# Performance work log

Hardware: AMD Instinct MI355X
Metric: run time of the kernel (lower is better)

## Reference

```python
import jax, jax.numpy as jnp
import numpy as np
from jax import lax

V_PATCH_NUMS = (1, 2, 3, 4, 5, 6, 8, 10, 13, 16)
SHARE_K = 4
RESI = 0.5  # abs(quant_resi)


def _area_matrix(pn, H):
    # F.interpolate(mode='area') == adaptive_avg_pool2d: uniform mean over [floor, ceil) window
    W = np.zeros((pn, H), np.float32)
    for i in range(pn):
        s = int(np.floor(i * H / pn)); e = int(np.ceil((i + 1) * H / pn))
        W[i, s:e] = 1.0 / (e - s)
    return W


def _cubic(x, a=-0.75):
    x = abs(x)
    if x <= 1.0:
        return (a + 2) * x**3 - (a + 3) * x**2 + 1
    if x < 2.0:
        return a * x**3 - 5 * a * x**2 + 8 * a * x - 4 * a
    return 0.0


def _bicubic_matrix(out, inp):
    # torch bicubic, align_corners=False, a=-0.75, border-clamped (separable 1D matrix)
    W = np.zeros((out, inp), np.float32)
    for i in range(out):
        src = (i + 0.5) * inp / out - 0.5
        i0 = int(np.floor(src)); t = src - i0
        for k in range(-1, 3):
            j = min(max(i0 + k, 0), inp - 1)
            W[i, j] += _cubic(k - t)
    return W


def _phi_select(si, SN, K=SHARE_K):
    ticks = np.linspace(1 / 3 / K, 1 - 1 / 3 / K, K) if K == 4 else np.linspace(1 / 2 / K, 1 - 1 / 2 / K, K)
    return int(np.argmin(np.abs(ticks - si / (SN - 1))))


def _phi(h, w, b):
    # Phi: h*(1-r) + conv3x3(h)*r
    y = lax.conv_general_dilated(h, w, (1, 1), 'SAME',
                                 dimension_numbers=('NCHW', 'OIHW', 'NCHW'))
    y = y + b[None, :, None, None]
    return h * (1.0 - RESI) + y * RESI


def reference(f, embedding, phi_w, phi_b):
    # Multi-scale residual vector quantization (VectorQuantizer2 hot path).
    # f: [B, C, 16, 16] latent; embedding: [V, C]; phi_w: [K, C, C, 3, 3]; phi_b: [K, C]
    B, C, H, Wd = f.shape
    SN = len(V_PATCH_NUMS)
    e2 = jnp.sum(embedding**2, axis=1)  # [V]
    f_hat = jnp.zeros_like(f)
    f_rest = f
    for si, pn in enumerate(V_PATCH_NUMS):
        if si != SN - 1:
            A = jnp.asarray(_area_matrix(pn, H))
            z = jnp.einsum('ph,bchw,qw->bcpq', A, f_rest, A)  # area downsample to pn x pn
        else:
            z = f_rest
        zf = z.transpose(0, 2, 3, 1).reshape(-1, C)  # [B*pn*pn, C]
        # squared-distance cdist + argmin codebook lookup
        d = jnp.sum(zf**2, axis=1, keepdims=True) - 2.0 * (zf @ embedding.T) + e2[None, :]
        idx = jnp.argmin(d, axis=1)  # [B*pn*pn]
        h = embedding[idx].reshape(B, pn, pn, C).transpose(0, 3, 1, 2)  # gather -> [B,C,pn,pn]
        if si != SN - 1:
            U = jnp.asarray(_bicubic_matrix(H, pn))
            h = jnp.einsum('hp,bcpq,wq->bchw', U, h, U)  # bicubic upsample to H x W
        k = _phi_select(si, SN)
        h = _phi(h, phi_w[k], phi_b[k])  # partially-shared Phi residual refinement
        f_hat = f_hat + h
        f_rest = f_rest - h
    return f_hat


def setup_inputs() -> dict:
    key = jax.random.key(0)
    k1, k2, k3 = jax.random.split(key, 3)
    f = jax.random.normal(k1, (64, 32, 16, 16), dtype=jnp.float32)
    embedding = jax.random.normal(k2, (4096, 32), dtype=jnp.float32)
    phi_w = jax.random.normal(k3, (4, 32, 32, 3, 3), dtype=jnp.float32) * 0.05
    phi_b = jnp.zeros((4, 32), dtype=jnp.float32)
    return {"f": f, "embedding": embedding, "phi_w": phi_w, "phi_b": phi_b}
```

## Files before the change

kernel.cpp:

```cpp
#include <hip/hip_runtime.h>
#include <cmath>


#define BB 64
#define CC 32
#define HH 16
#define VV 4096
#define NTOT (BB*CC*HH*HH)
#define ABASE 163840
#define ATOT  42624

typedef __attribute__((ext_vector_type(8))) short bf16x8;
typedef __attribute__((ext_vector_type(4))) float f32x4;

__device__ __forceinline__ double cubicw(double x) {
    x = fabs(x);
    const double a = -0.75;
    if (x <= 1.0) return ((a + 2.0) * x - (a + 3.0)) * x * x + 1.0;
    if (x < 2.0)  return (((a * x - 5.0 * a) * x + 8.0 * a) * x - 4.0 * a);
    return 0.0;
}

__device__ __forceinline__ unsigned int ordf(float d) {
    unsigned int b = __float_as_uint(d);
    return (b & 0x80000000u) ? ~b : (b | 0x80000000u);
}

__device__ __forceinline__ short f2bf(float x) {
    unsigned u = __float_as_uint(x);
    unsigned r = (u + 0x7fffu + ((u >> 16) & 1u)) >> 16;
    return (short)r;
}
__device__ __forceinline__ float bf2f(short h) {
    return __uint_as_float(((unsigned)(unsigned short)h) << 16);
}

__global__ void init_k(const float* __restrict__ f, const float* __restrict__ E,
                       float* __restrict__ f_rest,
                       float* __restrict__ e2, float* __restrict__ z,
                       unsigned short* __restrict__ est,
                       unsigned long long* __restrict__ bka) {
    int i = blockIdx.x * 256 + threadIdx.x;
    if (i < NTOT) f_rest[i] = f[i];
    if (bka && i < ATOT) bka[i] = ~0ull;
    if (i < VV) {
        float s = 0.f;
        int tile = i >> 4, n = i & 15;
        #pragma unroll
        for (int c = 0; c < CC; ++c) {
            float x = E[i * CC + c];
            s += x * x;
            if (est) {
                short h = f2bf(x); float rm = x - bf2f(h);
                short m = f2bf(rm); float rl = rm - bf2f(m);
                short l = f2bf(rl);
                int idx = tile * 1536 + (n * 4 + (c >> 3)) * 8 + (c & 7);
                est[idx]        = (unsigned short)h;
                est[idx + 512]  = (unsigned short)m;
                est[idx + 1024] = (unsigned short)l;
            }
        }
        e2[i] = s;
    }
    if (i < BB * CC) {
        const float* src = f + (size_t)i * (HH * HH);
        float s = 0.f;
        for (int j = 0; j < HH * HH; ++j) s += src[j];
        z[i] = s * (1.0f / 256.0f);
    }
}

__global__ __launch_bounds__(256, 4) void argsmall_k(const float* __restrict__ z,
        const float* __restrict__ E, const float* __restrict__ e2,
        unsigned long long* __restrict__ bestk, int M, int G, int gsz) {
    const int t = threadIdx.x;
    int m = blockIdx.x * 64 + (t & 63);
    int w = __builtin_amdgcn_readfirstlane(t >> 6);
    int wg = blockIdx.y * 4 + w;
    int v0 = wg * gsz;
    float zr[CC]; float z2 = 0.f;
    const float4* zp = (const float4*)(z + (size_t)m * CC);
    #pragma unroll
    for (int c4 = 0; c4 < 8; ++c4) {
        float4 v = zp[c4];
        zr[c4*4+0] = v.x; zr[c4*4+1] = v.y; zr[c4*4+2] = v.z; zr[c4*4+3] = v.w;
        z2 += v.x*v.x + v.y*v.y + v.z*v.z + v.w*v.w;
    }
    const float* e = E + (size_t)v0 * CC;
    float best = 3.4e38f; int bv = v0;
    for (int v = v0; v < v0 + gsz; v += 2, e += 2 * CC) {
        float a0 = 0.f, a1 = 0.f, b0 = 0.f, b1 = 0.f;
        #pragma unroll
        for (int c = 0; c < CC; c += 2) {
            a0 = fmaf(zr[c],   e[c],      a0);
            a1 = fmaf(zr[c+1], e[c+1],    a1);
            b0 = fmaf(zr[c],   e[CC+c],   b0);
            b1 = fmaf(zr[c+1], e[CC+c+1], b1);
        }
        float dA = fmaf(-2.f, a0 + a1, z2 + e2[v]);
        float dB = fmaf(-2.f, b0 + b1, z2 + e2[v+1]);
        if (dA < best) { best = dA; bv = v; }
        if (dB < best) { best = dB; bv = v + 1; }
    }
    bestk[(size_t)m * G + wg] = ((unsigned long long)ordf(best) << 32) |
                                (unsigned long long)(unsigned int)bv;
}

__global__ __launch_bounds__(256, 4) void argmf_k(const unsigned short* __restrict__ zs,
        const unsigned short* __restrict__ est, const float* __restrict__ e2,
        unsigned long long* __restrict__ bka, int M, int G, int gsz) {
    const int t = threadIdx.x;
    const int g = blockIdx.y;
    const int v0 = g * gsz;
    const int lane = t & 63;
    const int w = t >> 6;
    const int n = lane & 15, kq = lane >> 4;

    int tb[2]; bf16x8 ah[2], am[2], al[2];
    #pragma unroll
    for (int pt = 0; pt < 2; ++pt) {
        int tb0 = blockIdx.x * 128 + w * 32 + pt * 16;
        if (tb0 > M - 16) tb0 = M - 16;
        tb[pt] = tb0;
        const unsigned short* zp = zs + (size_t)(tb0 + n) * 96 + kq * 8;
        ah[pt] = *(const bf16x8*)(zp);
        am[pt] = *(const bf16x8*)(zp + 32);
        al[pt] = *(const bf16x8*)(zp + 64);
    }

    float bd[2][4]; int bc[2][4];
    #pragma unroll
    for (int pt = 0; pt < 2; ++pt)
        #pragma unroll
        for (int r = 0; r < 4; ++r) { bd[pt][r] = 3.4e38f; bc[pt][r] = 0; }

    const int nct = gsz >> 4;
    const unsigned short* ep = est + (size_t)(v0 >> 4) * 1536 +
                               (size_t)(n * 4 + kq) * 8;
    const float* e2p = e2 + v0 + n;
    bf16x8 eh = *(const bf16x8*)(ep);
    bf16x8 em = *(const bf16x8*)(ep + 512);
    bf16x8 el = *(const bf16x8*)(ep + 1024);
    float e2c = *e2p;
    for (int ct = 0; ct < nct; ++ct) {
        bf16x8 ceh = eh, cem = em, cel = el; float ce2 = e2c;
        if (ct + 1 < nct) {
            ep += 1536; e2p += 16;
            eh = *(const bf16x8*)(ep);
            em = *(const bf16x8*)(ep + 512);
            el = *(const bf16x8*)(ep + 1024);
            e2c = *e2p;
        }
        #pragma unroll
        for (int pt = 0; pt < 2; ++pt) {
            f32x4 Ca = {0.f, 0.f, 0.f, 0.f};
            f32x4 Cb = {ce2, ce2, ce2, ce2};
            Ca = __builtin_amdgcn_mfma_f32_16x16x32_bf16(ah[pt], ceh, Ca, 0, 0, 0);
            Cb = __builtin_amdgcn_mfma_f32_16x16x32_bf16(am[pt], ceh, Cb, 0, 0, 0);
            Ca = __builtin_amdgcn_mfma_f32_16x16x32_bf16(ah[pt], cem, Ca, 0, 0, 0);
            Cb = __builtin_amdgcn_mfma_f32_16x16x32_bf16(al[pt], ceh, Cb, 0, 0, 0);
            Ca = __builtin_amdgcn_mfma_f32_16x16x32_bf16(ah[pt], cel, Ca, 0, 0, 0);
            Cb = __builtin_amdgcn_mfma_f32_16x16x32_bf16(am[pt], cem, Cb, 0, 0, 0);
            #pragma unroll
            for (int r = 0; r < 4; ++r) {
                float d = Ca[r] + Cb[r];
                if (d < bd[pt][r]) { bd[pt][r] = d; bc[pt][r] = ct; }
            }
        }
    }
    #pragma unroll
    for (int pt = 0; pt < 2; ++pt) {
        #pragma unroll
        for (int r = 0; r < 4; ++r) {
            int v = v0 + bc[pt][r] * 16 + n;
            unsigned long long k = ((unsigned long long)ordf(bd[pt][r]) << 32) |
                                   (unsigned long long)(unsigned int)v;
            #pragma unroll
            for (int msk = 1; msk < 16; msk <<= 1) {
                unsigned long long o = __shfl_xor(k, msk);
                if (o < k) k = o;
            }
            if (n == 0)
                atomicMin(&bka[(size_t)(tb[pt] + kq * 4 + r)], k);
        }
    }
}

__global__ __launch_bounds__(256, 2) void argmf4_k(const unsigned short* __restrict__ zs,
        const unsigned short* __restrict__ est, const float* __restrict__ e2,
        unsigned long long* __restrict__ bka, int M, int G, int gsz) {
    const int t = threadIdx.x;
    const int g = blockIdx.y;
    const int v0 = g * gsz;
    const int lane = t & 63;
    const int w = t >> 6;
    const int n = lane & 15, kq = lane >> 4;

    int tb[4]; bf16x8 ah[4], am[4], al[4];
    #pragma unroll
    for (int pt = 0; pt < 4; ++pt) {
        int tb0 = blockIdx.x * 256 + w * 64 + pt * 16;
        if (tb0 > M - 16) tb0 = M - 16;
        tb[pt] = tb0;
        const unsigned short* zp = zs + (size_t)(tb0 + n) * 96 + kq * 8;
        ah[pt] = *(const bf16x8*)(zp);
        am[pt] = *(const bf16x8*)(zp + 32);
        al[pt] = *(const bf16x8*)(zp + 64);
    }

    float bd[4][4]; int bc[4][4];
    #pragma unroll
    for (int pt = 0; pt < 4; ++pt)
        #pragma unroll
        for (int r = 0; r < 4; ++r) { bd[pt][r] = 3.4e38f; bc[pt][r] = 0; }

    const int nct = gsz >> 4;
    const unsigned short* ep = est + (size_t)(v0 >> 4) * 1536 +
                               (size_t)(n * 4 + kq) * 8;
    const float* e2p = e2 + v0 + n;
    bf16x8 eh = *(const bf16x8*)(ep);
    bf16x8 em = *(const bf16x8*)(ep + 512);
    bf16x8 el = *(const bf16x8*)(ep + 1024);
    float e2c = *e2p;
    for (int ct = 0; ct < nct; ++ct) {
        bf16x8 ceh = eh, cem = em, cel = el; float ce2 = e2c;
        if (ct + 1 < nct) {
            ep += 1536; e2p += 16;
            eh = *(const bf16x8*)(ep);
            em = *(const bf16x8*)(ep + 512);
            el = *(const bf16x8*)(ep + 1024);
            e2c = *e2p;
        }
        #pragma unroll
        for (int pt = 0; pt < 4; ++pt) {
            f32x4 Ca = {0.f, 0.f, 0.f, 0.f};
            f32x4 Cb = {ce2, ce2, ce2, ce2};
            Ca = __builtin_amdgcn_mfma_f32_16x16x32_bf16(ah[pt], ceh, Ca, 0, 0, 0);
            Cb = __builtin_amdgcn_mfma_f32_16x16x32_bf16(am[pt], ceh, Cb, 0, 0, 0);
            Ca = __builtin_amdgcn_mfma_f32_16x16x32_bf16(ah[pt], cem, Ca, 0, 0, 0);
            Cb = __builtin_amdgcn_mfma_f32_16x16x32_bf16(al[pt], ceh, Cb, 0, 0, 0);
            Ca = __builtin_amdgcn_mfma_f32_16x16x32_bf16(ah[pt], cel, Ca, 0, 0, 0);
            Cb = __builtin_amdgcn_mfma_f32_16x16x32_bf16(am[pt], cem, Cb, 0, 0, 0);
            #pragma unroll
            for (int r = 0; r < 4; ++r) {
                float d = Ca[r] + Cb[r];
                if (d < bd[pt][r]) { bd[pt][r] = d; bc[pt][r] = ct; }
            }
        }
    }
    #pragma unroll
    for (int pt = 0; pt < 4; ++pt) {
        #pragma unroll
        for (int r = 0; r < 4; ++r) {
            int v = v0 + bc[pt][r] * 16 + n;
            unsigned long long k = ((unsigned long long)ordf(bd[pt][r]) << 32) |
                                   (unsigned long long)(unsigned int)v;
            #pragma unroll
            for (int msk = 1; msk < 16; msk <<= 1) {
                unsigned long long o = __shfl_xor(k, msk);
                if (o < k) k = o;
            }
            if (n == 0)
                atomicMin(&bka[(size_t)(tb[pt] + kq * 4 + r)], k);
        }
    }
}

__global__ __launch_bounds__(256, 4) void argbig_k(const float* __restrict__ z,
        const float* __restrict__ E, const float* __restrict__ e2,
        unsigned long long* __restrict__ bestk, int M, int G, int gsz) {
    __shared__ float s_e[128 * CC];
    __shared__ float s_e2[128];
    const int T = gridDim.x * 256;
    const int g = blockIdx.y;
    const int v0 = g * gsz;
    {
        const float4* src = (const float4*)(E + (size_t)v0 * CC);
        float4* dst = (float4*)s_e;
        for (int i = threadIdx.x; i < gsz * 8; i += 256) dst[i] = src[i];
        if (threadIdx.x < gsz) s_e2[threadIdx.x] = e2[v0 + threadIdx.x];
    }
    int   mm[2];
    bool  act[2];
    float zr[2][CC];
    float z2[2];
    #pragma unroll
    for (int pt = 0; pt < 2; ++pt) {
        int m0 = blockIdx.x * 256 + threadIdx.x + pt * T;
        act[pt] = (m0 < M);
        int m = act[pt] ? m0 : M - 1;
        mm[pt] = m;
        const float4* zp = (const float4*)(z + (size_t)m * CC);
        float zz = 0.f;
        #pragma unroll
        for (int c4 = 0; c4 < 8; ++c4) {
            float4 v = zp[c4];
            zr[pt][c4*4+0] = v.x; zr[pt][c4*4+1] = v.y;
            zr[pt][c4*4+2] = v.z; zr[pt][c4*4+3] = v.w;
            zz += v.x*v.x + v.y*v.y + v.z*v.z + v.w*v.w;
        }
        z2[pt] = zz;
    }
    __syncthreads();
    float best[2]; int bv[2];
    #pragma unroll
    for (int pt = 0; pt < 2; ++pt) { best[pt] = 3.4e38f; bv[pt] = v0; }
    const float4* ev = (const float4*)s_e;
    for (int vi = 0; vi < gsz; ++vi, ev += 8) {
        float4 e0 = ev[0], e1 = ev[1], e2v = ev[2], e3 = ev[3];
        float4 e4 = ev[4], e5 = ev[5], e6v = ev[6], e7 = ev[7];
        float ef[CC] = {e0.x,e0.y,e0.z,e0.w, e1.x,e1.y,e1.z,e1.w,
                        e2v.x,e2v.y,e2v.z,e2v.w, e3.x,e3.y,e3.z,e3.w,
                        e4.x,e4.y,e4.z,e4.w, e5.x,e5.y,e5.z,e5.w,
                        e6v.x,e6v.y,e6v.z,e6v.w, e7.x,e7.y,e7.z,e7.w};
        float a0 = 0.f, a1 = 0.f, b0 = 0.f, b1 = 0.f;
        #pragma unroll
        for (int c = 0; c < CC; c += 2) {
            a0 = fmaf(zr[0][c],   ef[c],   a0);
            a1 = fmaf(zr[0][c+1], ef[c+1], a1);
            b0 = fmaf(zr[1][c],   ef[c],   b0);
            b1 = fmaf(zr[1][c+1], ef[c+1], b1);
        }
        float e2c = s_e2[vi];
        float dA = fmaf(-2.f, a0 + a1, z2[0] + e2c);
        float dB = fmaf(-2.f, b0 + b1, z2[1] + e2c);
        int v = v0 + vi;
        if (dA < best[0]) { best[0] = dA; bv[0] = v; }
        if (dB < best[1]) { best[1] = dB; bv[1] = v; }
    }
    #pragma unroll
    for (int pt = 0; pt < 2; ++pt)
        if (act[pt])
            bestk[(size_t)mm[pt] * G + g] =
                ((unsigned long long)ordf(best[pt]) << 32) |
                (unsigned long long)(unsigned int)bv[pt];
}

__global__ __launch_bounds__(512) void fuse_k(const unsigned long long* __restrict__ bestk,
                      const float* __restrict__ E,
                      const float* __restrict__ pw, const float* __restrict__ pb,
                      const float* __restrict__ fsrc, float* __restrict__ fout,
                      float* __restrict__ f_rest,
                      float* __restrict__ z_next, unsigned short* __restrict__ zsn,
                      int pn, int G, int TPP, int kphi, int pnn) {
    __shared__ float s_buf[CC * 18 * 20];
    __shared__ float s_scratch[256 * 36];
    __shared__ float s_pw[CC * 3 * 4 * 8];
    __shared__ int   s_idx[256];
    __shared__ float s_w[HH][4];
    __shared__ int   s_j[HH][4];
    __shared__ unsigned long long s_red[256];
    const int t   = threadIdx.x;
    const int cog = blockIdx.x;
    const int b   = blockIdx.y;
    const int P   = pn * pn;
    const int half = t >> 8;
    const int tl   = t & 255;

    if (G == 0) {
        if (t < P)
            s_idx[t] = (int)(unsigned int)(bestk[(size_t)b * P + t] & 0xffffffffull);
    } else {
        int p = t / TPP, sub = t - p * TPP;
        unsigned long long bk = ~0ull;
        if (p < P) {
            const unsigned long long* kp = bestk + (size_t)(b * P + p) * G;
            for (int gg = sub; gg < G; gg += TPP) {
                unsigned long long o = kp[gg];
                if (o < bk) bk = o;
            }
        }
        int bfly = TPP > 64 ? 64 : TPP;
        for (int msk = 1; msk < bfly; msk <<= 1) {
            unsigned long long o = __shfl_xor(bk, msk);
            if (o < bk) bk = o;
        }
        if (p < P) {
            if (TPP <= 64) {
                if (sub == 0) s_red[p] = bk;
            } else {
                int K = TPP >> 6;
                if ((sub & 63) == 0) s_red[p * K + (sub >> 6)] = bk;
            }
        }
    }
    if (t < HH) {
        double src = (t + 0.5) * (double)pn / 16.0 - 0.5;
        double fi = floor(src); int i0 = (int)fi; double tt = src - fi;
        #pragma unroll
        for (int k = 0; k < 4; ++k) {
            int j = i0 - 1 + k; j = j < 0 ? 0 : (j > pn - 1 ? pn - 1 : j);
            s_j[t][k] = j;
            s_w[t][k] = (float)cubicw((double)(k - 1) - tt);
        }
    }
    {
        const float* src = pw + ((size_t)(kphi * CC + cog * 8)) * CC * 9;
        for (int i = t; i < 8 * CC * 9; i += 512) {
            int l  = i / (CC * 9);
            int r  = i - l * (CC * 9);
            int ci = r / 9; int kk = r - ci * 9;
            int kh = kk / 3; int kw = kk - kh * 3;
            int cp = l >> 1, ce = l & 1;
            s_pw[ci * 96 + kh * 32 + cp * 8 + ce * 4 + kw] = src[i];
        }
    }
    __syncthreads();
    if (G != 0 && t < P) {
        unsigned long long r = s_red[(TPP <= 64) ? t : t * (TPP >> 6)];
        if (TPP > 64) {
            int K = TPP >> 6;
            for (int j2 = 1; j2 < K; ++j2) {
                unsigned long long o = s_red[t * K + j2];
                if (o < r) r = o;
            }
        }
        s_idx[t] = (int)(unsigned int)(r & 0xffffffffull);
    }
    if (G != 0) __syncthreads();

    if (tl < HH * pn) {
        int h = tl / pn, q = tl % pn;
        int cbase = half * 16;
        float acc[16];
        #pragma unroll
        for (int c = 0; c < 16; ++c) acc[c] = 0.f;
        #pragma unroll
        for (int k = 0; k < 4; ++k) {
            float wv = s_w[h][k];
            if (wv == 0.0f) continue;
            int row = s_idx[s_j[h][k] * pn + q];
            const float4* er = (const float4*)(E + (size_t)row * CC + cbase);
            #pragma unroll
            for (int c4 = 0; c4 < 4; ++c4) {
                float4 e4 = er[c4];
                acc[c4*4+0] = fmaf(wv, e4.x, acc[c4*4+0]);
                acc[c4*4+1] = fmaf(wv, e4.y, acc[c4*4+1]);
                acc[c4*4+2] = fmaf(wv, e4.z, acc[c4*4+2]);
                acc[c4*4+3] = fmaf(wv, e4.w, acc[c4*4+3]);
            }
        }
        float* dst = &s_scratch[(h * pn + q) * 36 + cbase];
        *(float4*)(dst + 0)  = make_float4(acc[0],  acc[1],  acc[2],  acc[3]);
        *(float4*)(dst + 4)  = make_float4(acc[4],  acc[5],  acc[6],  acc[7]);
        *(float4*)(dst + 8)  = make_float4(acc[8],  acc[9],  acc[10], acc[11]);
        *(float4*)(dst + 12) = make_float4(acc[12], acc[13], acc[14], acc[15]);
    }
    __syncthreads();

    {
        int h = tl >> 4, w = tl & 15;
        int cbase = half * 16;
        float acc[16];
        #pragma unroll
        for (int c = 0; c < 16; ++c) acc[c] = 0.f;
        #pragma unroll
        for (int k = 0; k < 4; ++k) {
            float wh = s_w[w][k];
            int j = s_j[w][k];
            const float4* sp4 = (const float4*)&s_scratch[(h * pn + j) * 36 + cbase];
            float4 v0 = sp4[0], v1 = sp4[1], v2 = sp4[2], v3 = sp4[3];
            acc[0]  = fmaf(wh, v0.x, acc[0]);  acc[1]  = fmaf(wh, v0.y, acc[1]);
            acc[2]  = fmaf(wh, v0.z, acc[2]);  acc[3]  = fmaf(wh, v0.w, acc[3]);
            acc[4]  = fmaf(wh, v1.x, acc[4]);  acc[5]  = fmaf(wh, v1.y, acc[5]);
            acc[6]  = fmaf(wh, v1.z, acc[6]);  acc[7]  = fmaf(wh, v1.w, acc[7]);
            acc[8]  = fmaf(wh, v2.x, acc[8]);  acc[9]  = fmaf(wh, v2.y, acc[9]);
            acc[10] = fmaf(wh, v2.z, acc[10]); acc[11] = fmaf(wh, v2.w, acc[11]);
            acc[12] = fmaf(wh, v3.x, acc[12]); acc[13] = fmaf(wh, v3.y, acc[13]);
            acc[14] = fmaf(wh, v3.z, acc[14]); acc[15] = fmaf(wh, v3.w, acc[15]);
        }
        #pragma unroll
        for (int c = 0; c < 16; ++c)
            s_buf[((cbase + c) * 18 + h + 1) * 20 + w + 1] = acc[c];
        if (w == 0) {
            #pragma unroll
            for (int c = 0; c < 16; ++c) s_buf[((cbase + c) * 18 + h + 1) * 20] = 0.f;
        }
        if (w >= 13) {
            #pragma unroll
            for (int c = 0; c < 16; ++c) s_buf[((cbase + c) * 18 + h + 1) * 20 + w + 4] = 0.f;
        }
        if (h == 0) {
            #pragma unroll
            for (int c = 0; c < 16; ++c) {
                s_buf[((cbase + c) * 18) * 20 + w] = 0.f;
                if (w < 4) s_buf[((cbase + c) * 18) * 20 + 16 + w] = 0.f;
            }
        }
        if (h == 15) {
            #pragma unroll
            for (int c = 0; c < 16; ++c) {
                s_buf[((cbase + c) * 18 + 17) * 20 + w] = 0.f;
                if (w < 4) s_buf[((cbase + c) * 18 + 17) * 20 + 16 + w] = 0.f;
            }
        }
    }
    __syncthreads();

    const int wave = t >> 6;
    const int lane = t & 63;
    const int cp   = ((wave & 1) << 1) | (lane >> 5);
    const int s    = lane & 31;
    const int h    = s >> 1;
    const int w0   = (s & 1) * 8;
    const int wid  = wave >> 1;
    const int pos  = cp * 32 + s;
    const int stag = wave & 1;
    float accE[8], accO[8];
    #pragma unroll
    for (int o = 0; o < 8; ++o) { accE[o] = 0.f; accO[o] = 0.f; }
    const int ci0 = wid * 8;
    for (int ci = ci0; ci < ci0 + 8; ++ci) {
        const float* wrow = &s_pw[ci * 96 + cp * 8];
        #pragma unroll
        for (int kk = 0; kk < 3; ++kk) {
            int kh = kk + stag; kh = (kh >= 3) ? kh - 3 : kh;
            const float4* xr = (const float4*)&s_buf[(ci * 18 + h + kh) * 20 + w0];
            float4 a0 = xr[0], a1 = xr[1], a2 = xr[2];
            float xf[12] = {a0.x, a0.y, a0.z, a0.w, a1.x, a1.y, a1.z, a1.w,
                            a2.x, a2.y, a2.z, a2.w};
            const float4* wp = (const float4*)(wrow + kh * 32);
            float4 wA = wp[0];
            float4 wB = wp[1];
            #pragma unroll
            for (int o = 0; o < 8; ++o) {
                accE[o] += xf[o] * wA.x + xf[o+1] * wA.y + xf[o+2] * wA.z;
                accO[o] += xf[o] * wB.x + xf[o+1] * wB.y + xf[o+2] * wB.z;
            }
        }
    }
    if (wid != 0) {
        float* dst = &s_scratch[((wid - 1) * 128 + pos) * 20];
        *(float4*)(dst +  0) = make_float4(accE[0], accE[1], accE[2], accE[3]);
        *(float4*)(dst +  4) = make_float4(accE[4], accE[5], accE[6], accE[7]);
        *(float4*)(dst +  8) = make_float4(accO[0], accO[1], accO[2], accO[3]);
        *(float4*)(dst + 12) = make_float4(accO[4], accO[5], accO[6], accO[7]);
    }
    __syncthreads();

    float4 rE0, rE1, rO0, rO1;
    if (wid == 0) {
        #pragma unroll
        for (int g2 = 0; g2 < 3; ++g2) {
            const float* sp = &s_scratch[(g2 * 128 + pos) * 20];
            float4 p0 = *(const float4*)(sp + 0), p1 = *(const float4*)(sp + 4);
            float4 p2 = *(const float4*)(sp + 8), p3 = *(const float4*)(sp + 12);
            accE[0] += p0.x; accE[1] += p0.y; accE[2] += p0.z; accE[3] += p0.w;
            accE[4] += p1.x; accE[5] += p1.y; accE[6] += p1.z; accE[7] += p1.w;
            accO[0] += p2.x; accO[1] += p2.y; accO[2] += p2.z; accO[3] += p2.w;
            accO[4] += p3.x; accO[5] += p3.y; accO[6] += p3.z; accO[7] += p3.w;
        }
        float biasE = pb[kphi * CC + cog * 8 + cp * 2];
        float biasO = pb[kphi * CC + cog * 8 + cp * 2 + 1];
        #pragma unroll
        for (int o = 0; o < 8; ++o) { accE[o] += biasE; accO[o] += biasO; }
        #pragma unroll
        for (int c = 0; c < 2; ++c) {
            const float* acc = c ? accO : accE;
            int co = cog * 8 + cp * 2 + c;
            float hf[8];
            #pragma unroll
            for (int o = 0; o < 8; ++o) {
                float hv = s_buf[(co * 18 + h + 1) * 20 + w0 + o + 1];
                hf[o] = 0.5f * hv + 0.5f * acc[o];
            }
            size_t base = ((size_t)(b * CC + co) * HH + h) * HH + w0;
            float4* fr = (float4*)(f_rest + base);
            float4 r0 = fr[0], r1 = fr[1];
            r0.x -= hf[0]; r0.y -= hf[1]; r0.z -= hf[2]; r0.w -= hf[3];
            r1.x -= hf[4]; r1.y -= hf[5]; r1.z -= hf[6]; r1.w -= hf[7];
            if (pnn > 0) {
                fr[0] = r0; fr[1] = r1;
            } else {
                const float4* fs = (const float4*)(fsrc + base);
                float4 s0 = fs[0], s1 = fs[1];
                float4 o0, o1;
                o0.x = s0.x - r0.x; o0.y = s0.y - r0.y;
                o0.z = s0.z - r0.z; o0.w = s0.w - r0.w;
                o1.x = s1.x - r1.x; o1.y = s1.y - r1.y;
                o1.z = s1.z - r1.z; o1.w = s1.w - r1.w;
                float4* fo = (float4*)(fout + base);
                fo[0] = o0; fo[1] = o1;
            }
            if (c) { rO0 = r0; rO1 = r1; } else { rE0 = r0; rE1 = r1; }
        }
    }

    if (pnn > 0) {
        __syncthreads();
        float* fn = s_buf;
        if (wid == 0) {
            #pragma unroll
            for (int c = 0; c < 2; ++c) {
                int cl = cp * 2 + c;
                float* d = &fn[(cl * HH + h) * HH + w0];
                float4 r0 = c ? rO0 : rE0, r1 = c ? rO1 : rE1;
                d[0] = r0.x; d[1] = r0.y; d[2] = r0.z; d[3] = r0.w;
                d[4] = r1.x; d[5] = r1.y; d[6] = r1.z; d[7] = r1.w;
            }
        }
        __syncthreads();
        int P2 = pnn * pnn;
        for (int i = t; i < P2 * 8; i += 512) {
            int cl = i & 7, pq = i >> 3;
            int q2 = pq % pnn, p2 = pq / pnn;
            int sp = (p2 * HH) / pnn, ep = ((p2 + 1) * HH + pnn - 1) / pnn;
            int sq = (q2 * HH) / pnn, eq = ((q2 + 1) * HH + pnn - 1) / pnn;
            float wgt = 1.0f / ((float)(ep - sp) * (float)(eq - sq));
            float sum = 0.f;
            for (int h2 = sp; h2 < ep; ++h2)
                for (int w2 = sq; w2 < eq; ++w2)
                    sum += fn[(cl * HH + h2) * HH + w2];
            float v = sum * wgt;
            int c = cog * 8 + cl;
            if (zsn) {
                float tv = -2.0f * v;
                size_t baz = (size_t)(b * P2 + pq) * 96 + c;
                unsigned short hh = (unsigned short)f2bf(tv);
                float rm = tv - bf2f((short)hh);
                unsigned short mm2 = (unsigned short)f2bf(rm);
                float rl = rm - bf2f((short)mm2);
                unsigned short ll = (unsigned short)f2bf(rl);
                zsn[baz] = hh; zsn[baz + 32] = mm2; zsn[baz + 64] = ll;
            } else {
                z_next[((size_t)(b * P2 + pq)) * CC + c] = v;
            }
        }
    }
}

extern "C" void kernel_launch(void* const* d_in, const int* in_sizes, int n_in,
                              void* d_out, int out_size, void* d_ws, size_t ws_size,
                              hipStream_t stream) {
    const float* f  = (const float*)d_in[0];
    const float* E  = (const float*)d_in[1];
    const float* pw = (const float*)d_in[2];
    const float* pb = (const float*)d_in[3];
    float* out = (float*)d_out;

    const size_t need_base = (size_t)(NTOT + VV) * 4 + (size_t)524288 * 8 +
                             (size_t)524288 * 4;
    const size_t need_mf = need_base + (size_t)VV * 96 * 2 +
                           (size_t)16384 * 96 * 2;
    const bool use_mf = (ws_size >= need_mf);

    float* wsf    = (float*)d_ws;
    float* f_rest = wsf;
    float* e2     = wsf + (size_t)NTOT;
    unsigned long long* bestk = (unsigned long long*)(e2 + VV);
    float* z      = (float*)(bestk + 524288);
    unsigned short* est = use_mf ? (unsigned short*)(z + 524288) : (unsigned short*)0;
    unsigned short* zs  = use_mf ? (est + (size_t)VV * 96) : (unsigned short*)0;
    unsigned long long* bka = use_mf ? (bestk + ABASE) : (unsigned long long*)0;

    int phik[10];
    {
        double start = 1.0 / 3.0 / 4.0;
        double stop  = 1.0 - 1.0 / 3.0 / 4.0;
        double step  = (stop - start) / 3.0;
        double ticks[4];
        for (int i = 0; i < 4; ++i) ticks[i] = (double)i * step + start;
        ticks[3] = stop;
        for (int si = 0; si < 10; ++si) {
            double s = (double)si / 9.0;
            int bk = 0; double bd = fabs(ticks[0] - s);
            for (int tq = 1; tq < 4; ++tq) {
                double d2 = fabs(ticks[tq] - s);
                if (d2 < bd) { bd = d2; bk = tq; }
            }
            phik[si] = bk;
        }
    }

    static const int pns[10]  = {1, 2, 3, 4, 5, 6, 8, 10, 13, 16};
    static const int grpS[10] = {256, 128, 64, 32, 32, 16, 0, 0, 0, 0};
    static const int grpF[10] = {0, 0, 0, 0, 0, 0, 128, 64, 32, 32};
    static const int grpM[10] = {0, 0, 0, 32, 32, 32, 16, 16, 16, 16};
    static const int aoff[10] = {0, 0, 0, 0, 1024, 2624, 4928, 9024, 15424, 26240};

    init_k<<<(NTOT + 255) / 256, 256, 0, stream>>>(f, E, f_rest, e2, z, est, bka);

    for (int si = 0; si < 10; ++si) {
        int pn = pns[si];
        int P = pn * pn;
        int M = BB * P;
        int G, TPP;
        bool small_path = use_mf ? (pn <= 3) : (pn <= 6);
        const unsigned long long* fuse_bk = bestk;
        if (small_path) {
            int grp = grpS[si];
            G = grp * 4;
            int gsz = VV / G;
            argsmall_k<<<dim3(P, grp), 256, 0, stream>>>(z, E, e2, bestk, M, G, gsz);
            TPP = 1;
            while (TPP * 2 * P <= 512) TPP *= 2;
        } else if (use_mf) {
            int grp = grpM[si];
            int gsz = VV / grp;
            unsigned long long* slice = bka + aoff[si];
            if (pn >= 8) {
                int bx = (M + 255) / 256;
                argmf4_k<<<dim3(bx, grp), 256, 0, stream>>>(zs, est, e2, slice, M, grp, gsz);
            } else {
                int bx = (M + 127) / 128;
                argmf_k<<<dim3(bx, grp), 256, 0, stream>>>(zs, est, e2, slice, M, grp, gsz);
            }
            fuse_bk = slice;
            G = 0; TPP = 1;
        } else {
            G = grpF[si];
            int gsz = VV / G;
            int bx = (M + 511) / 512;
            argbig_k<<<dim3(bx, G), 256, 0, stream>>>(z, E, e2, bestk, M, G, gsz);
            TPP = 1;
            while (TPP * 2 * P <= 512) TPP *= 2;
        }
        int pnn = (si < 9) ? pns[si + 1] : 0;
        unsigned short* zsn = (pnn >= 4 && use_mf) ? zs : (unsigned short*)0;
        fuse_k<<<dim3(4, BB), 512, 0, stream>>>(fuse_bk, E, pw, pb,
                                                f, out, f_rest, z, zsn,
                                                pn, G, TPP, phik[si], pnn);
    }
}
```

Measured before the change: 363.7 us.

## Fuse small-scale codebook argmin into fuse kernel with ping-pong z buffers

For scales with pn<=4 on the MFMA path, the separate argmin kernel launch is dropped. The fuse kernel now computes full codebook distances itself, with each block scanning all 4096 entries per patch position and reducing with shuffles. The z buffer is split into two halves used alternately, so a fuse block can read the current z while writing the next scale's z. This removes several kernel launches and global round-trips. In exchange, each of the 4x64 fuse blocks redundantly evaluates the whole codebook, leaving the small-scale argmin with far less parallelism than the dedicated kernel had.

```diff
diff --git a/kernel.cpp b/kernel.cpp
--- a/kernel.cpp
+++ b/kernel.cpp
@@ -341,6 +341,7 @@
                       const float* __restrict__ pw, const float* __restrict__ pb,
                       const float* __restrict__ fsrc, float* __restrict__ fout,
                       float* __restrict__ f_rest,
+                      const float* __restrict__ z_in, const float* __restrict__ e2g,
                       float* __restrict__ z_next, unsigned short* __restrict__ zsn,
                       int pn, int G, int TPP, int kphi, int pnn) {
     __shared__ float s_buf[CC * 18 * 20];
@@ -360,6 +361,46 @@
     if (G == 0) {
         if (t < P)
             s_idx[t] = (int)(unsigned int)(bestk[(size_t)b * P + t] & 0xffffffffull);
+    } else if (G < 0) {
+        int p = t / TPP, sub = t - p * TPP;
+        unsigned long long bk = ~0ull;
+        if (p < P) {
+            float zr[CC]; float z2 = 0.f;
+            const float4* zp4 = (const float4*)(z_in + (size_t)(b * P + p) * CC);
+            #pragma unroll
+            for (int c4 = 0; c4 < 8; ++c4) {
+                float4 v4 = zp4[c4];
+                zr[c4*4+0] = v4.x; zr[c4*4+1] = v4.y;
+                zr[c4*4+2] = v4.z; zr[c4*4+3] = v4.w;
+                z2 += v4.x*v4.x + v4.y*v4.y + v4.z*v4.z + v4.w*v4.w;
+            }
+            const float* e = E + (size_t)sub * CC;
+            for (int v = sub; v < VV; v += TPP, e += (size_t)TPP * CC) {
+                float a0 = 0.f, a1 = 0.f;
+                #pragma unroll
+                for (int c = 0; c < CC; c += 2) {
+                    a0 = fmaf(zr[c],   e[c],   a0);
+                    a1 = fmaf(zr[c+1], e[c+1], a1);
+                }
+                float dA = fmaf(-2.f, a0 + a1, z2 + e2g[v]);
+                unsigned long long k = ((unsigned long long)ordf(dA) << 32) |
+                                       (unsigned long long)(unsigned int)v;
+                if (k < bk) bk = k;
+            }
+        }
+        int bfly = TPP > 64 ? 64 : TPP;
+        for (int msk = 1; msk < bfly; msk <<= 1) {
+            unsigned long long o = __shfl_xor(bk, msk);
+            if (o < bk) bk = o;
+        }
+        if (p < P) {
+            if (TPP <= 64) {
+                if (sub == 0) s_red[p] = bk;
+            } else {
+                int K = TPP >> 6;
+                if ((sub & 63) == 0) s_red[p * K + (sub >> 6)] = bk;
+            }
+        }
     } else {
         int p = t / TPP, sub = t - p * TPP;
         unsigned long long bk = ~0ull;
@@ -649,6 +690,8 @@
     float* e2     = wsf + (size_t)NTOT;
     unsigned long long* bestk = (unsigned long long*)(e2 + VV);
     float* z      = (float*)(bestk + 524288);
+    float* zA     = z;
+    float* zB     = z + 262144;
     unsigned short* est = use_mf ? (unsigned short*)(z + 524288) : (unsigned short*)0;
     unsigned short* zs  = use_mf ? (est + (size_t)VV * 96) : (unsigned short*)0;
     unsigned long long* bka = use_mf ? (bestk + ABASE) : (unsigned long long*)0;
@@ -675,23 +718,21 @@
     static const int pns[10]  = {1, 2, 3, 4, 5, 6, 8, 10, 13, 16};
     static const int grpS[10] = {256, 128, 64, 32, 32, 16, 0, 0, 0, 0};
     static const int grpF[10] = {0, 0, 0, 0, 0, 0, 128, 64, 32, 32};
-    static const int grpM[10] = {0, 0, 0, 32, 32, 32, 16, 16, 16, 16};
+    static const int grpM[10] = {0, 0, 0, 0, 32, 32, 16, 16, 16, 16};
     static const int aoff[10] = {0, 0, 0, 0, 1024, 2624, 4928, 9024, 15424, 26240};
 
-    init_k<<<(NTOT + 255) / 256, 256, 0, stream>>>(f, E, f_rest, e2, z, est, bka);
+    init_k<<<(NTOT + 255) / 256, 256, 0, stream>>>(f, E, f_rest, e2, zA, est, bka);
 
     for (int si = 0; si < 10; ++si) {
         int pn = pns[si];
         int P = pn * pn;
         int M = BB * P;
         int G, TPP;
-        bool small_path = use_mf ? (pn <= 3) : (pn <= 6);
         const unsigned long long* fuse_bk = bestk;
-        if (small_path) {
-            int grp = grpS[si];
-            G = grp * 4;
-            int gsz = VV / G;
-            argsmall_k<<<dim3(P, grp), 256, 0, stream>>>(z, E, e2, bestk, M, G, gsz);
+        const float* zin = use_mf ? ((si & 1) ? zB : zA) : zA;
+        float* zout      = use_mf ? ((si & 1) ? zA : zB) : zA;
+        if (use_mf && pn <= 4) {
+            G = -1;
             TPP = 1;
             while (TPP * 2 * P <= 512) TPP *= 2;
         } else if (use_mf) {
@@ -707,18 +748,26 @@
             }
             fuse_bk = slice;
             G = 0; TPP = 1;
+        } else if (pn <= 6) {
+            int grp = grpS[si];
+            G = grp * 4;
+            int gsz = VV / G;
+            argsmall_k<<<dim3(P, grp), 256, 0, stream>>>(zA, E, e2, bestk, M, G, gsz);
+            TPP = 1;
+            while (TPP * 2 * P <= 512) TPP *= 2;
         } else {
             G = grpF[si];
             int gsz = VV / G;
             int bx = (M + 511) / 512;
-            argbig_k<<<dim3(bx, G), 256, 0, stream>>>(z, E, e2, bestk, M, G, gsz);
+            argbig_k<<<dim3(bx, G), 256, 0, stream>>>(zA, E, e2, bestk, M, G, gsz);
             TPP = 1;
             while (TPP * 2 * P <= 512) TPP *= 2;
         }
         int pnn = (si < 9) ? pns[si + 1] : 0;
-        unsigned short* zsn = (pnn >= 4 && use_mf) ? zs : (unsigned short*)0;
+        unsigned short* zsn = (pnn >= 5 && use_mf) ? zs : (unsigned short*)0;
         fuse_k<<<dim3(4, BB), 512, 0, stream>>>(fuse_bk, E, pw, pb,
-                                                f, out, f_rest, z, zsn,
+                                                f, out, f_rest,
+                                                zin, e2, zout, zsn,
                                                 pn, G, TPP, phik[si], pnn);
     }
 }
```

After: 752.7 us. +107.0%, slower.

## Shrink fuse_k LDS and registers; split conv so each thread owns one output channel

Applied to the files above, without the earlier changes.

Splits the bicubic upsample into two 16-channel passes using a smaller shared scratch buffer, and aliases the reduction buffer onto it. The 3x3 Phi conv is remapped so each thread computes 4 outputs of one channel over all 32 input channels, which removes the cross-wave partial-sum reduction and its barrier. It also adds a minimum-blocks hint to launch_bounds so more blocks fit per CU. The aim is higher occupancy and less shared-memory traffic, at the cost of an extra barrier pair in the upsample and longer serial loops per thread.

```diff
diff --git a/kernel.cpp b/kernel.cpp
--- a/kernel.cpp
+++ b/kernel.cpp
@@ -336,7 +336,7 @@
                 (unsigned long long)(unsigned int)bv[pt];
 }
 
-__global__ __launch_bounds__(512) void fuse_k(const unsigned long long* __restrict__ bestk,
+__global__ __launch_bounds__(512, 4) void fuse_k(const unsigned long long* __restrict__ bestk,
                       const float* __restrict__ E,
                       const float* __restrict__ pw, const float* __restrict__ pb,
                       const float* __restrict__ fsrc, float* __restrict__ fout,
@@ -344,12 +344,12 @@
                       float* __restrict__ z_next, unsigned short* __restrict__ zsn,
                       int pn, int G, int TPP, int kphi, int pnn) {
     __shared__ float s_buf[CC * 18 * 20];
-    __shared__ float s_scratch[256 * 36];
+    __shared__ __align__(16) float s_vert[256 * 20];
     __shared__ float s_pw[CC * 3 * 4 * 8];
     __shared__ int   s_idx[256];
     __shared__ float s_w[HH][4];
     __shared__ int   s_j[HH][4];
-    __shared__ unsigned long long s_red[256];
+    unsigned long long* s_red = (unsigned long long*)s_vert;
     const int t   = threadIdx.x;
     const int cog = blockIdx.x;
     const int b   = blockIdx.y;
@@ -419,186 +419,135 @@
     }
     if (G != 0) __syncthreads();
 
-    if (tl < HH * pn) {
-        int h = tl / pn, q = tl % pn;
-        int cbase = half * 16;
-        float acc[16];
-        #pragma unroll
-        for (int c = 0; c < 16; ++c) acc[c] = 0.f;
-        #pragma unroll
-        for (int k = 0; k < 4; ++k) {
-            float wv = s_w[h][k];
-            if (wv == 0.0f) continue;
-            int row = s_idx[s_j[h][k] * pn + q];
-            const float4* er = (const float4*)(E + (size_t)row * CC + cbase);
-            #pragma unroll
-            for (int c4 = 0; c4 < 4; ++c4) {
-                float4 e4 = er[c4];
-                acc[c4*4+0] = fmaf(wv, e4.x, acc[c4*4+0]);
-                acc[c4*4+1] = fmaf(wv, e4.y, acc[c4*4+1]);
-                acc[c4*4+2] = fmaf(wv, e4.z, acc[c4*4+2]);
-                acc[c4*4+3] = fmaf(wv, e4.w, acc[c4*4+3]);
-            }
-        }
-        float* dst = &s_scratch[(h * pn + q) * 36 + cbase];
-        *(float4*)(dst + 0)  = make_float4(acc[0],  acc[1],  acc[2],  acc[3]);
-        *(float4*)(dst + 4)  = make_float4(acc[4],  acc[5],  acc[6],  acc[7]);
-        *(float4*)(dst + 8)  = make_float4(acc[8],  acc[9],  acc[10], acc[11]);
-        *(float4*)(dst + 12) = make_float4(acc[12], acc[13], acc[14], acc[15]);
-    }
-    __syncthreads();
-
-    {
-        int h = tl >> 4, w = tl & 15;
-        int cbase = half * 16;
-        float acc[16];
-        #pragma unroll
-        for (int c = 0; c < 16; ++c) acc[c] = 0.f;
-        #pragma unroll
-        for (int k = 0; k < 4; ++k) {
-            float wh = s_w[w][k];
-            int j = s_j[w][k];
-            const float4* sp4 = (const float4*)&s_scratch[(h * pn + j) * 36 + cbase];
-            float4 v0 = sp4[0], v1 = sp4[1], v2 = sp4[2], v3 = sp4[3];
-            acc[0]  = fmaf(wh, v0.x, acc[0]);  acc[1]  = fmaf(wh, v0.y, acc[1]);
-            acc[2]  = fmaf(wh, v0.z, acc[2]);  acc[3]  = fmaf(wh, v0.w, acc[3]);
-            acc[4]  = fmaf(wh, v1.x, acc[4]);  acc[5]  = fmaf(wh, v1.y, acc[5]);
-            acc[6]  = fmaf(wh, v1.z, acc[6]);  acc[7]  = fmaf(wh, v1.w, acc[7]);
-            acc[8]  = fmaf(wh, v2.x, acc[8]);  acc[9]  = fmaf(wh, v2.y, acc[9]);
-            acc[10] = fmaf(wh, v2.z, acc[10]); acc[11] = fmaf(wh, v2.w, acc[11]);
-            acc[12] = fmaf(wh, v3.x, acc[12]); acc[13] = fmaf(wh, v3.y, acc[13]);
-            acc[14] = fmaf(wh, v3.z, acc[14]); acc[15] = fmaf(wh, v3.w, acc[15]);
-        }
-        #pragma unroll
-        for (int c = 0; c < 16; ++c)
-            s_buf[((cbase + c) * 18 + h + 1) * 20 + w + 1] = acc[c];
-        if (w == 0) {
-            #pragma unroll
-            for (int c = 0; c < 16; ++c) s_buf[((cbase + c) * 18 + h + 1) * 20] = 0.f;
-        }
-        if (w >= 13) {
-            #pragma unroll
-            for (int c = 0; c < 16; ++c) s_buf[((cbase + c) * 18 + h + 1) * 20 + w + 4] = 0.f;
-        }
-        if (h == 0) {
-            #pragma unroll
-            for (int c = 0; c < 16; ++c) {
-                s_buf[((cbase + c) * 18) * 20 + w] = 0.f;
-                if (w < 4) s_buf[((cbase + c) * 18) * 20 + 16 + w] = 0.f;
-            }
-        }
-        if (h == 15) {
-            #pragma unroll
-            for (int c = 0; c < 16; ++c) {
-                s_buf[((cbase + c) * 18 + 17) * 20 + w] = 0.f;
-                if (w < 4) s_buf[((cbase + c) * 18 + 17) * 20 + 16 + w] = 0.f;
-            }
-        }
-    }
-    __syncthreads();
+    #pragma unroll
+    for (int p = 0; p < 2; ++p) {
+        const int cbase = p * 16 + half * 8;
+        if (tl < HH * pn) {
+            int h = tl / pn, q = tl % pn;
+            float acc[8];
+            #pragma unroll
+            for (int c = 0; c < 8; ++c) acc[c] = 0.f;
+            #pragma unroll
+            for (int k = 0; k < 4; ++k) {
+                float wv = s_w[h][k];
+                if (wv == 0.0f) continue;
+                int row = s_idx[s_j[h][k] * pn + q];
+                const float4* er = (const float4*)(E + (size_t)row * CC + cbase);
+                float4 e0 = er[0], e1 = er[1];
+                acc[0] = fmaf(wv, e0.x, acc[0]); acc[1] = fmaf(wv, e0.y, acc[1]);
+                acc[2] = fmaf(wv, e0.z, acc[2]); acc[3] = fmaf(wv, e0.w, acc[3]);
+                acc[4] = fmaf(wv, e1.x, acc[4]); acc[5] = fmaf(wv, e1.y, acc[5]);
+                acc[6] = fmaf(wv, e1.z, acc[6]); acc[7] = fmaf(wv, e1.w, acc[7]);
+            }
+            float* dst = &s_vert[(h * pn + q) * 20 + half * 8];
+            *(float4*)(dst + 0) = make_float4(acc[0], acc[1], acc[2], acc[3]);
+            *(float4*)(dst + 4) = make_float4(acc[4], acc[5], acc[6], acc[7]);
+        }
+        __syncthreads();
+        {
+            int h = tl >> 4, w = tl & 15;
+            float acc[8];
+            #pragma unroll
+            for (int c = 0; c < 8; ++c) acc[c] = 0.f;
+            #pragma unroll
+            for (int k = 0; k < 4; ++k) {
+                float wh = s_w[w][k];
+                int j = s_j[w][k];
+                const float4* sp4 = (const float4*)&s_vert[(h * pn + j) * 20 + half * 8];
+                float4 v0 = sp4[0], v1 = sp4[1];
+                acc[0] = fmaf(wh, v0.x, acc[0]); acc[1] = fmaf(wh, v0.y, acc[1]);
+                acc[2] = fmaf(wh, v0.z, acc[2]); acc[3] = fmaf(wh, v0.w, acc[3]);
+                acc[4] = fmaf(wh, v1.x, acc[4]); acc[5] = fmaf(wh, v1.y, acc[5]);
+                acc[6] = fmaf(wh, v1.z, acc[6]); acc[7] = fmaf(wh, v1.w, acc[7]);
+            }
+            #pragma unroll
+            for (int c = 0; c < 8; ++c)
+                s_buf[((cbase + c) * 18 + h + 1) * 20 + w + 1] = acc[c];
+            if (w == 0) {
+                #pragma unroll
+                for (int c = 0; c < 8; ++c) s_buf[((cbase + c) * 18 + h + 1) * 20] = 0.f;
+            }
+            if (w >= 13) {
+                #pragma unroll
+                for (int c = 0; c < 8; ++c) s_buf[((cbase + c) * 18 + h + 1) * 20 + w + 4] = 0.f;
+            }
+            if (h == 0) {
+                #pragma unroll
+                for (int c = 0; c < 8; ++c) {
+                    s_buf[((cbase + c) * 18) * 20 + w] = 0.f;
+                    if (w < 4) s_buf[((cbase + c) * 18) * 20 + 16 + w] = 0.f;
+                }
+            }
+            if (h == 15) {
+                #pragma unroll
+                for (int c = 0; c < 8; ++c) {
+                    s_buf[((cbase + c) * 18 + 17) * 20 + w] = 0.f;
+                    if (w < 4) s_buf[((cbase + c) * 18 + 17) * 20 + 16 + w] = 0.f;
+                }
+            }
+        }
+        __syncthreads();
+    }
 
     const int wave = t >> 6;
     const int lane = t & 63;
-    const int cp   = ((wave & 1) << 1) | (lane >> 5);
-    const int s    = lane & 31;
-    const int h    = s >> 1;
-    const int w0   = (s & 1) * 8;
-    const int wid  = wave >> 1;
-    const int pos  = cp * 32 + s;
+    const int coL  = lane >> 4;
+    const int low  = lane & 15;
+    const int co   = (wave >> 2) * 4 + coL;
+    const int h    = (wave & 3) * 4 + (low >> 2);
+    const int wq   = low & 3;
+    const int w0   = wq * 4;
+    const int cp   = co >> 1, ce = co & 1;
     const int stag = wave & 1;
-    float accE[8], accO[8];
-    #pragma unroll
-    for (int o = 0; o < 8; ++o) { accE[o] = 0.f; accO[o] = 0.f; }
-    const int ci0 = wid * 8;
-    for (int ci = ci0; ci < ci0 + 8; ++ci) {
-        const float* wrow = &s_pw[ci * 96 + cp * 8];
+    float acc[4] = {0.f, 0.f, 0.f, 0.f};
+    for (int ci = 0; ci < CC; ++ci) {
         #pragma unroll
         for (int kk = 0; kk < 3; ++kk) {
             int kh = kk + stag; kh = (kh >= 3) ? kh - 3 : kh;
             const float4* xr = (const float4*)&s_buf[(ci * 18 + h + kh) * 20 + w0];
-            float4 a0 = xr[0], a1 = xr[1], a2 = xr[2];
-            float xf[12] = {a0.x, a0.y, a0.z, a0.w, a1.x, a1.y, a1.z, a1.w,
-                            a2.x, a2.y, a2.z, a2.w};
-            const float4* wp = (const float4*)(wrow + kh * 32);
-            float4 wA = wp[0];
-            float4 wB = wp[1];
-            #pragma unroll
-            for (int o = 0; o < 8; ++o) {
-                accE[o] += xf[o] * wA.x + xf[o+1] * wA.y + xf[o+2] * wA.z;
-                accO[o] += xf[o] * wB.x + xf[o+1] * wB.y + xf[o+2] * wB.z;
-            }
-        }
-    }
-    if (wid != 0) {
-        float* dst = &s_scratch[((wid - 1) * 128 + pos) * 20];
-        *(float4*)(dst +  0) = make_float4(accE[0], accE[1], accE[2], accE[3]);
-        *(float4*)(dst +  4) = make_float4(accE[4], accE[5], accE[6], accE[7]);
-        *(float4*)(dst +  8) = make_float4(accO[0], accO[1], accO[2], accO[3]);
-        *(float4*)(dst + 12) = make_float4(accO[4], accO[5], accO[6], accO[7]);
-    }
-    __syncthreads();
-
-    float4 rE0, rE1, rO0, rO1;
-    if (wid == 0) {
-        #pragma unroll
-        for (int g2 = 0; g2 < 3; ++g2) {
-            const float* sp = &s_scratch[(g2 * 128 + pos) * 20];
-            float4 p0 = *(const float4*)(sp + 0), p1 = *(const float4*)(sp + 4);
-            float4 p2 = *(const float4*)(sp + 8), p3 = *(const float4*)(sp + 12);
-            accE[0] += p0.x; accE[1] += p0.y; accE[2] += p0.z; accE[3] += p0.w;
-            accE[4] += p1.x; accE[5] += p1.y; accE[6] += p1.z; accE[7] += p1.w;
-            accO[0] += p2.x; accO[1] += p2.y; accO[2] += p2.z; accO[3] += p2.w;
-            accO[4] += p3.x; accO[5] += p3.y; accO[6] += p3.z; accO[7] += p3.w;
-        }
-        float biasE = pb[kphi * CC + cog * 8 + cp * 2];
-        float biasO = pb[kphi * CC + cog * 8 + cp * 2 + 1];
-        #pragma unroll
-        for (int o = 0; o < 8; ++o) { accE[o] += biasE; accO[o] += biasO; }
-        #pragma unroll
-        for (int c = 0; c < 2; ++c) {
-            const float* acc = c ? accO : accE;
-            int co = cog * 8 + cp * 2 + c;
-            float hf[8];
-            #pragma unroll
-            for (int o = 0; o < 8; ++o) {
-                float hv = s_buf[(co * 18 + h + 1) * 20 + w0 + o + 1];
-                hf[o] = 0.5f * hv + 0.5f * acc[o];
-            }
-            size_t base = ((size_t)(b * CC + co) * HH + h) * HH + w0;
-            float4* fr = (float4*)(f_rest + base);
-            float4 r0 = fr[0], r1 = fr[1];
-            r0.x -= hf[0]; r0.y -= hf[1]; r0.z -= hf[2]; r0.w -= hf[3];
-            r1.x -= hf[4]; r1.y -= hf[5]; r1.z -= hf[6]; r1.w -= hf[7];
-            if (pnn > 0) {
-                fr[0] = r0; fr[1] = r1;
-            } else {
-                const float4* fs = (const float4*)(fsrc + base);
-                float4 s0 = fs[0], s1 = fs[1];
-                float4 o0, o1;
-                o0.x = s0.x - r0.x; o0.y = s0.y - r0.y;
-                o0.z = s0.z - r0.z; o0.w = s0.w - r0.w;
-                o1.x = s1.x - r1.x; o1.y = s1.y - r1.y;
-                o1.z = s1.z - r1.z; o1.w = s1.w - r1.w;
-                float4* fo = (float4*)(fout + base);
-                fo[0] = o0; fo[1] = o1;
-            }
-            if (c) { rO0 = r0; rO1 = r1; } else { rE0 = r0; rE1 = r1; }
+            float4 a0 = xr[0], a1 = xr[1];
+            float xf[6] = {a0.x, a0.y, a0.z, a0.w, a1.x, a1.y};
+            float4 wv = *(const float4*)&s_pw[ci * 96 + kh * 32 + cp * 8 + ce * 4];
+            #pragma unroll
+            for (int o = 0; o < 4; ++o)
+                acc[o] += xf[o] * wv.x + xf[o+1] * wv.y + xf[o+2] * wv.z;
+        }
+    }
+    {
+        float bias = pb[kphi * CC + cog * 8 + co];
+        #pragma unroll
+        for (int o = 0; o < 4; ++o) acc[o] += bias;
+    }
+
+    float4 r0;
+    {
+        const int cg = cog * 8 + co;
+        float hf[4];
+        #pragma unroll
+        for (int o = 0; o < 4; ++o) {
+            float hv = s_buf[(cg * 18 + h + 1) * 20 + w0 + o + 1];
+            hf[o] = 0.5f * hv + 0.5f * acc[o];
+        }
+        size_t base = ((size_t)(b * CC + cg) * HH + h) * HH + w0;
+        float4* fr = (float4*)(f_rest + base);
+        r0 = fr[0];
+        r0.x -= hf[0]; r0.y -= hf[1]; r0.z -= hf[2]; r0.w -= hf[3];
+        if (pnn > 0) {
+            fr[0] = r0;
+        } else {
+            const float4* fs = (const float4*)(fsrc + base);
+            float4 s0 = fs[0];
+            float4 o0;
+            o0.x = s0.x - r0.x; o0.y = s0.y - r0.y;
+            o0.z = s0.z - r0.z; o0.w = s0.w - r0.w;
+            *(float4*)(fout + base) = o0;
         }
     }
 
     if (pnn > 0) {
         __syncthreads();
         float* fn = s_buf;
-        if (wid == 0) {
-            #pragma unroll
-            for (int c = 0; c < 2; ++c) {
-                int cl = cp * 2 + c;
-                float* d = &fn[(cl * HH + h) * HH + w0];
-                float4 r0 = c ? rO0 : rE0, r1 = c ? rO1 : rE1;
-                d[0] = r0.x; d[1] = r0.y; d[2] = r0.z; d[3] = r0.w;
-                d[4] = r1.x; d[5] = r1.y; d[6] = r1.z; d[7] = r1.w;
-            }
-        }
+        *(float4*)&fn[(co * HH + h) * HH + w0] = r0;
         __syncthreads();
         int P2 = pnn * pnn;
         for (int i = t; i < P2 * 8; i += 512) {
```

Result: slower. 483.7 us (+33.0%).
